# Optimization experiments

Measured on AMD Instinct MI355X. Metric: run time of the kernel, lower is better.

## Reference

```python
import jax, jax.numpy as jnp
import numpy as np

T, B, D = 4096, 64, 64
SCALE = D ** (-0.5)


def setup_inputs() -> dict:
    key = jax.random.key(0)
    ks = jax.random.split(key, 8)
    init = 1.0 / np.sqrt(D)  # mimic nn.Linear default scale roughly
    return {
        "eeg": jax.random.normal(ks[0], (T, B, D), dtype=jnp.float32),
        "fnirs": jax.random.normal(ks[1], (T, B, D), dtype=jnp.float32),
        "Wq": jax.random.normal(ks[2], (D, D), dtype=jnp.float32) * init,
        "bq": jax.random.normal(ks[3], (D,), dtype=jnp.float32) * init,
        "Wk": jax.random.normal(ks[4], (D, D), dtype=jnp.float32) * init,
        "bk": jax.random.normal(ks[5], (D,), dtype=jnp.float32) * init,
        "Wv": jax.random.normal(ks[6], (D, D), dtype=jnp.float32) * init,
        "bv": jax.random.normal(ks[7], (D,), dtype=jnp.float32) * init,
    }


def reference(eeg, fnirs, Wq, bq, Wk, bk, Wv, bv):
    # Linear layers: x @ W.T + b (torch nn.Linear convention, W is [out, in])
    q = jnp.einsum("tbd,od->tbo", eeg, Wq) + bq      # [T, B, D]
    k = jnp.einsum("tbd,od->tbo", fnirs, Wk) + bk    # [T, B, D]
    v = jnp.einsum("tbd,od->tbo", fnirs, Wv) + bv    # [T, B, D]
    # Elementwise QK gating score, summed over feature dim -> [T, B, 1]
    score = jnp.sum(q * k, axis=-1, keepdims=True) * SCALE
    # Softmax over the sequence axis (dim=0)
    attn = jax.nn.softmax(score, axis=0)
    # Residual combine
    return eeg + attn * v
```

## Files before the change

### kernel.cpp

```cpp
#include <hip/hip_runtime.h>
#include <hip/hip_bf16.h>
#include <math.h>

#define T_DIM 4096
#define B_DIM 64
#define D_DIM 64
#define NROWS (T_DIM * B_DIM)
#define NTILES (NROWS / 16)

#define WS_MBF   0
#define WS_VBF   2048
#define WS_UBF   4096
#define WS_W     4160
#define WS_C     4224
#define WS_SCORE 8192

typedef __attribute__((ext_vector_type(4))) float f32x4;
typedef __attribute__((ext_vector_type(8))) short bf16x8;

static __device__ inline short f2bf(float x) {
  __hip_bfloat16 h = __float2bfloat16(x);
  return *reinterpret_cast<short*>(&h);
}

static __device__ inline bf16x8 cvt8(const float4 a, const float4 b) {
  bf16x8 r;
  r[0] = f2bf(a.x); r[1] = f2bf(a.y); r[2] = f2bf(a.z); r[3] = f2bf(a.w);
  r[4] = f2bf(b.x); r[5] = f2bf(b.y); r[6] = f2bf(b.z); r[7] = f2bf(b.w);
  return r;
}

__global__ __launch_bounds__(64) void k1_precompute(
    const float* __restrict__ Wq, const float* __restrict__ bq,
    const float* __restrict__ Wk, const float* __restrict__ bk,
    const float* __restrict__ Wv, float* __restrict__ ws) {
  const int tid = threadIdx.x;
  const int blk = blockIdx.x;
  unsigned short* __restrict__ mbf = (unsigned short*)(ws + WS_MBF);
  unsigned short* __restrict__ vbf = (unsigned short*)(ws + WS_VBF);
  unsigned short* __restrict__ ubf = (unsigned short*)(ws + WS_UBF);
  if (blk < 64) {
    const int d = blk;
    float acc = 0.f;
    for (int o = 0; o < 64; ++o)
      acc = fmaf(Wq[o * 64 + d], Wk[o * 64 + tid], acc);
    mbf[d * 64 + tid] = (unsigned short)f2bf(acc);
    vbf[d * 64 + tid] = (unsigned short)f2bf(Wv[d * 64 + tid]);
  } else {
    float uacc = 0.f, wacc = 0.f, cacc = 0.f;
    for (int o = 0; o < 64; ++o) {
      uacc = fmaf(bq[o], Wk[o * 64 + tid], uacc);
      wacc = fmaf(Wq[o * 64 + tid], bk[o], wacc);
      cacc = fmaf(bq[o], bk[o], cacc);
    }
    ubf[tid] = (unsigned short)f2bf(uacc);
    ws[WS_W + tid] = wacc;
    if (tid == 0) ws[WS_C] = cacc;
  }
}

__global__ __launch_bounds__(256, 4) void k2_score_mfma(
    const float* __restrict__ eeg, const float* __restrict__ fnirs,
    const unsigned short* __restrict__ mbf, const float* __restrict__ wvec,
    const unsigned short* __restrict__ ubf, const float* __restrict__ cvec,
    float* __restrict__ score) {
  const int lane = threadIdx.x & 63;
  const int wv   = threadIdx.x >> 6;
  const int tile = blockIdx.x * 4 + wv;
  const int col  = lane & 15;
  const int grp  = lane >> 4;
  const int kb   = grp * 8;
  const int rbase = tile * 16;

  const float* fa = fnirs + (size_t)(rbase + col) * 64 + kb;
  const float4 f0a = *reinterpret_cast<const float4*>(fa);
  const float4 f0b = *reinterpret_cast<const float4*>(fa + 4);
  const float4 f1a = *reinterpret_cast<const float4*>(fa + 32);
  const float4 f1b = *reinterpret_cast<const float4*>(fa + 36);
  float ee[4][4];
#pragma unroll
  for (int i = 0; i < 4; ++i)
#pragma unroll
    for (int ct = 0; ct < 4; ++ct)
      ee[i][ct] = eeg[(size_t)(rbase + grp * 4 + i) * 64 + ct * 16 + col];

  bf16x8 bm[5][2];
#pragma unroll
  for (int ct = 0; ct < 4; ++ct)
#pragma unroll
    for (int kf = 0; kf < 2; ++kf)
      bm[ct][kf] = *reinterpret_cast<const bf16x8*>(
          mbf + (ct * 16 + col) * 64 + kf * 32 + kb);
#pragma unroll
  for (int kf = 0; kf < 2; ++kf) {
    bf16x8 z = (bf16x8)(short)0;
    if (col == 0)
      z = *reinterpret_cast<const bf16x8*>(ubf + kf * 32 + kb);
    bm[4][kf] = z;
  }
  const float wreg[4] = { wvec[col], wvec[16 + col], wvec[32 + col], wvec[48 + col] };
  const float cb = cvec[0];

  const bf16x8 a0 = cvt8(f0a, f0b);
  const bf16x8 a1 = cvt8(f1a, f1b);
  const f32x4 zero = {0.f, 0.f, 0.f, 0.f};
  f32x4 acc[5];
#pragma unroll
  for (int ct = 0; ct < 5; ++ct) {
    acc[ct] = __builtin_amdgcn_mfma_f32_16x16x32_bf16(a0, bm[ct][0], zero, 0, 0, 0);
    acc[ct] = __builtin_amdgcn_mfma_f32_16x16x32_bf16(a1, bm[ct][1], acc[ct], 0, 0, 0);
  }

  float partial[4];
#pragma unroll
  for (int i = 0; i < 4; ++i) {
    float s = 0.f;
#pragma unroll
    for (int ct = 0; ct < 4; ++ct)
      s = fmaf(ee[i][ct], acc[ct][i] + wreg[ct], s);
    if (col == 0) s += acc[4][i] + cb;
    partial[i] = s;
  }
#pragma unroll
  for (int m = 8; m >= 1; m >>= 1)
#pragma unroll
    for (int i = 0; i < 4; ++i)
      partial[i] += __shfl_xor(partial[i], m, 64);
  if (col == 0) {
    float4 o = { partial[0] * 0.125f, partial[1] * 0.125f,
                 partial[2] * 0.125f, partial[3] * 0.125f };
    *reinterpret_cast<float4*>(score + rbase + grp * 4) = o;
  }
}

__global__ __launch_bounds__(256) void k3_softmax(float* __restrict__ sc) {
  __shared__ float red[8];
  __shared__ float sinv;
  const int b = blockIdx.x;
  const int tid = threadIdx.x;

  float vals[16];
  float m = -1e30f;
#pragma unroll
  for (int k = 0; k < 16; ++k) {
    vals[k] = sc[(size_t)(k * 256 + tid) * 64 + b];
    m = fmaxf(m, vals[k]);
  }
#pragma unroll
  for (int off = 32; off > 0; off >>= 1)
    m = fmaxf(m, __shfl_xor(m, off, 64));
  if ((tid & 63) == 0) red[tid >> 6] = m;
  __syncthreads();
  m = fmaxf(fmaxf(red[0], red[1]), fmaxf(red[2], red[3]));

  float s = 0.f;
#pragma unroll
  for (int k = 0; k < 16; ++k) s += __expf(vals[k] - m);
#pragma unroll
  for (int off = 32; off > 0; off >>= 1)
    s += __shfl_xor(s, off, 64);
  if ((tid & 63) == 0) red[4 + (tid >> 6)] = s;
  __syncthreads();
  if (tid == 0) sinv = 1.0f / (red[4] + red[5] + red[6] + red[7]);
  __syncthreads();
  const float inv = sinv;
#pragma unroll
  for (int k = 0; k < 16; ++k)
    sc[(size_t)(k * 256 + tid) * 64 + b] = __expf(vals[k] - m) * inv;
}

__global__ __launch_bounds__(256, 4) void k4_output_mfma(
    const float* __restrict__ eeg, const float* __restrict__ fnirs,
    const unsigned short* __restrict__ vbf, const float* __restrict__ bv,
    const float* __restrict__ attn, float* __restrict__ out) {
  const int lane = threadIdx.x & 63;
  const int wv   = threadIdx.x >> 6;
  const int tile = blockIdx.x * 4 + wv;
  const int col  = lane & 15;
  const int grp  = lane >> 4;
  const int kb   = grp * 8;
  const int rbase = tile * 16;

  const float* fa = fnirs + (size_t)(rbase + col) * 64 + kb;
  const float4 f0a = *reinterpret_cast<const float4*>(fa);
  const float4 f0b = *reinterpret_cast<const float4*>(fa + 4);
  const float4 f1a = *reinterpret_cast<const float4*>(fa + 32);
  const float4 f1b = *reinterpret_cast<const float4*>(fa + 36);
  float ee[4][4];
#pragma unroll
  for (int i = 0; i < 4; ++i)
#pragma unroll
    for (int ct = 0; ct < 4; ++ct)
      ee[i][ct] = eeg[(size_t)(rbase + grp * 4 + i) * 64 + ct * 16 + col];
  const float4 a4 = *reinterpret_cast<const float4*>(attn + rbase + grp * 4);

  bf16x8 bm[4][2];
#pragma unroll
  for (int ct = 0; ct < 4; ++ct)
#pragma unroll
    for (int kf = 0; kf < 2; ++kf)
      bm[ct][kf] = *reinterpret_cast<const bf16x8*>(
          vbf + (ct * 16 + col) * 64 + kf * 32 + kb);
  const float bvreg[4] = { bv[col], bv[16 + col], bv[32 + col], bv[48 + col] };

  const bf16x8 a0 = cvt8(f0a, f0b);
  const bf16x8 a1 = cvt8(f1a, f1b);
  const f32x4 zero = {0.f, 0.f, 0.f, 0.f};
  f32x4 acc[4];
#pragma unroll
  for (int ct = 0; ct < 4; ++ct) {
    acc[ct] = __builtin_amdgcn_mfma_f32_16x16x32_bf16(a0, bm[ct][0], zero, 0, 0, 0);
    acc[ct] = __builtin_amdgcn_mfma_f32_16x16x32_bf16(a1, bm[ct][1], acc[ct], 0, 0, 0);
  }

  const float av[4] = { a4.x, a4.y, a4.z, a4.w };
#pragma unroll
  for (int i = 0; i < 4; ++i) {
    const size_t row = rbase + grp * 4 + i;
#pragma unroll
    for (int ct = 0; ct < 4; ++ct)
      out[row * 64 + ct * 16 + col] = fmaf(av[i], acc[ct][i] + bvreg[ct], ee[i][ct]);
  }
}

extern "C" void kernel_launch(void* const* d_in, const int* in_sizes, int n_in,
                              void* d_out, int out_size, void* d_ws, size_t ws_size,
                              hipStream_t stream) {
  const float* eeg   = (const float*)d_in[0];
  const float* fnirs = (const float*)d_in[1];
  const float* Wq    = (const float*)d_in[2];
  const float* bq    = (const float*)d_in[3];
  const float* Wk    = (const float*)d_in[4];
  const float* bk    = (const float*)d_in[5];
  const float* Wv    = (const float*)d_in[6];
  const float* bv    = (const float*)d_in[7];
  float* out = (float*)d_out;
  float* ws  = (float*)d_ws;

  k1_precompute<<<65, 64, 0, stream>>>(Wq, bq, Wk, bk, Wv, ws);
  k2_score_mfma<<<NTILES / 4, 256, 0, stream>>>(
      eeg, fnirs,
      (const unsigned short*)(ws + WS_MBF), ws + WS_W,
      (const unsigned short*)(ws + WS_UBF), ws + WS_C, ws + WS_SCORE);
  k3_softmax<<<64, 256, 0, stream>>>(ws + WS_SCORE);
  k4_output_mfma<<<NTILES / 4, 256, 0, stream>>>(
      eeg, fnirs, (const unsigned short*)(ws + WS_VBF), bv,
      ws + WS_SCORE, out);
}
```

Baseline: 79.63 us.

## Split softmax into parallel partial reductions and vectorize eeg/out access via transposed MFMA

The single 64-block softmax kernel becomes a 512-block online max/sum partial pass plus a tiny combine kernel. Normalization (exp and scale) moves into the output kernel, so the normalized attention no longer has to be written back. The MFMA operands are swapped so each lane owns one row and gets contiguous columns, which lets eeg loads and output stores use float4 and replaces the 16-lane shuffle reduction with two shuffles. The u bias term is now an fp32 dot product instead of an extra bf16 MFMA tile. The cost is one more kernel launch and one extra exp per row in the output kernel.

After: 87.48 us. +9.9%, slower.

```diff
diff --git a/kernel.cpp b/kernel.cpp
--- a/kernel.cpp
+++ b/kernel.cpp
@@ -10,9 +10,12 @@
 
 #define WS_MBF   0
 #define WS_VBF   2048
-#define WS_UBF   4096
+#define WS_U     4096
 #define WS_W     4160
 #define WS_C     4224
+#define WS_MX    4240
+#define WS_INV   4304
+#define WS_PART  4368
 #define WS_SCORE 8192
 
 typedef __attribute__((ext_vector_type(4))) float f32x4;
@@ -28,6 +31,12 @@
   r[0] = f2bf(a.x); r[1] = f2bf(a.y); r[2] = f2bf(a.z); r[3] = f2bf(a.w);
   r[4] = f2bf(b.x); r[5] = f2bf(b.y); r[6] = f2bf(b.z); r[7] = f2bf(b.w);
   return r;
+}
+
+static __device__ inline float dot4(const float4 a, const float4 b, float acc) {
+  acc = fmaf(a.x, b.x, acc); acc = fmaf(a.y, b.y, acc);
+  acc = fmaf(a.z, b.z, acc); acc = fmaf(a.w, b.w, acc);
+  return acc;
 }
 
 __global__ __launch_bounds__(64) void k1_precompute(
@@ -38,7 +47,6 @@
   const int blk = blockIdx.x;
   unsigned short* __restrict__ mbf = (unsigned short*)(ws + WS_MBF);
   unsigned short* __restrict__ vbf = (unsigned short*)(ws + WS_VBF);
-  unsigned short* __restrict__ ubf = (unsigned short*)(ws + WS_UBF);
   if (blk < 64) {
     const int d = blk;
     float acc = 0.f;
@@ -53,7 +61,7 @@
       wacc = fmaf(Wq[o * 64 + tid], bk[o], wacc);
       cacc = fmaf(bq[o], bk[o], cacc);
     }
-    ubf[tid] = (unsigned short)f2bf(uacc);
+    ws[WS_U + tid] = uacc;
     ws[WS_W + tid] = wacc;
     if (tid == 0) ws[WS_C] = cacc;
   }
@@ -62,7 +70,7 @@
 __global__ __launch_bounds__(256, 4) void k2_score_mfma(
     const float* __restrict__ eeg, const float* __restrict__ fnirs,
     const unsigned short* __restrict__ mbf, const float* __restrict__ wvec,
-    const unsigned short* __restrict__ ubf, const float* __restrict__ cvec,
+    const float* __restrict__ uvec, const float* __restrict__ cvec,
     float* __restrict__ score) {
   const int lane = threadIdx.x & 63;
   const int wv   = threadIdx.x >> 6;
@@ -77,102 +85,117 @@
   const float4 f0b = *reinterpret_cast<const float4*>(fa + 4);
   const float4 f1a = *reinterpret_cast<const float4*>(fa + 32);
   const float4 f1b = *reinterpret_cast<const float4*>(fa + 36);
-  float ee[4][4];
-#pragma unroll
-  for (int i = 0; i < 4; ++i)
-#pragma unroll
-    for (int ct = 0; ct < 4; ++ct)
-      ee[i][ct] = eeg[(size_t)(rbase + grp * 4 + i) * 64 + ct * 16 + col];
-
-  bf16x8 bm[5][2];
-#pragma unroll
-  for (int ct = 0; ct < 4; ++ct)
+  const float* ea = eeg + (size_t)(rbase + col) * 64 + grp * 4;
+  const float4 ef0 = *reinterpret_cast<const float4*>(ea);
+  const float4 ef1 = *reinterpret_cast<const float4*>(ea + 16);
+  const float4 ef2 = *reinterpret_cast<const float4*>(ea + 32);
+  const float4 ef3 = *reinterpret_cast<const float4*>(ea + 48);
+
+  bf16x8 bm[4][2];
+#pragma unroll
+  for (int dt = 0; dt < 4; ++dt)
 #pragma unroll
     for (int kf = 0; kf < 2; ++kf)
-      bm[ct][kf] = *reinterpret_cast<const bf16x8*>(
-          mbf + (ct * 16 + col) * 64 + kf * 32 + kb);
-#pragma unroll
-  for (int kf = 0; kf < 2; ++kf) {
-    bf16x8 z = (bf16x8)(short)0;
-    if (col == 0)
-      z = *reinterpret_cast<const bf16x8*>(ubf + kf * 32 + kb);
-    bm[4][kf] = z;
-  }
-  const float wreg[4] = { wvec[col], wvec[16 + col], wvec[32 + col], wvec[48 + col] };
+      bm[dt][kf] = *reinterpret_cast<const bf16x8*>(
+          mbf + (dt * 16 + col) * 64 + kf * 32 + kb);
+  const float4 wf0 = *reinterpret_cast<const float4*>(wvec + 0  + grp * 4);
+  const float4 wf1 = *reinterpret_cast<const float4*>(wvec + 16 + grp * 4);
+  const float4 wf2 = *reinterpret_cast<const float4*>(wvec + 32 + grp * 4);
+  const float4 wf3 = *reinterpret_cast<const float4*>(wvec + 48 + grp * 4);
+  const float4 u0a = *reinterpret_cast<const float4*>(uvec + kb);
+  const float4 u0b = *reinterpret_cast<const float4*>(uvec + kb + 4);
+  const float4 u1a = *reinterpret_cast<const float4*>(uvec + kb + 32);
+  const float4 u1b = *reinterpret_cast<const float4*>(uvec + kb + 36);
   const float cb = cvec[0];
+
+  float s = 0.f;
+  s = dot4(f0a, u0a, s); s = dot4(f0b, u0b, s);
+  s = dot4(f1a, u1a, s); s = dot4(f1b, u1b, s);
 
   const bf16x8 a0 = cvt8(f0a, f0b);
   const bf16x8 a1 = cvt8(f1a, f1b);
   const f32x4 zero = {0.f, 0.f, 0.f, 0.f};
-  f32x4 acc[5];
-#pragma unroll
-  for (int ct = 0; ct < 5; ++ct) {
-    acc[ct] = __builtin_amdgcn_mfma_f32_16x16x32_bf16(a0, bm[ct][0], zero, 0, 0, 0);
-    acc[ct] = __builtin_amdgcn_mfma_f32_16x16x32_bf16(a1, bm[ct][1], acc[ct], 0, 0, 0);
-  }
-
-  float partial[4];
-#pragma unroll
-  for (int i = 0; i < 4; ++i) {
-    float s = 0.f;
-#pragma unroll
-    for (int ct = 0; ct < 4; ++ct)
-      s = fmaf(ee[i][ct], acc[ct][i] + wreg[ct], s);
-    if (col == 0) s += acc[4][i] + cb;
-    partial[i] = s;
-  }
-#pragma unroll
-  for (int m = 8; m >= 1; m >>= 1)
-#pragma unroll
-    for (int i = 0; i < 4; ++i)
-      partial[i] += __shfl_xor(partial[i], m, 64);
-  if (col == 0) {
-    float4 o = { partial[0] * 0.125f, partial[1] * 0.125f,
-                 partial[2] * 0.125f, partial[3] * 0.125f };
-    *reinterpret_cast<float4*>(score + rbase + grp * 4) = o;
-  }
-}
-
-__global__ __launch_bounds__(256) void k3_softmax(float* __restrict__ sc) {
-  __shared__ float red[8];
-  __shared__ float sinv;
-  const int b = blockIdx.x;
+  f32x4 acc[4];
+#pragma unroll
+  for (int dt = 0; dt < 4; ++dt) {
+    acc[dt] = __builtin_amdgcn_mfma_f32_16x16x32_bf16(bm[dt][0], a0, zero, 0, 0, 0);
+    acc[dt] = __builtin_amdgcn_mfma_f32_16x16x32_bf16(bm[dt][1], a1, acc[dt], 0, 0, 0);
+  }
+
+  float4 h;
+  h.x = acc[0][0] + wf0.x; h.y = acc[0][1] + wf0.y; h.z = acc[0][2] + wf0.z; h.w = acc[0][3] + wf0.w;
+  s = dot4(ef0, h, s);
+  h.x = acc[1][0] + wf1.x; h.y = acc[1][1] + wf1.y; h.z = acc[1][2] + wf1.z; h.w = acc[1][3] + wf1.w;
+  s = dot4(ef1, h, s);
+  h.x = acc[2][0] + wf2.x; h.y = acc[2][1] + wf2.y; h.z = acc[2][2] + wf2.z; h.w = acc[2][3] + wf2.w;
+  s = dot4(ef2, h, s);
+  h.x = acc[3][0] + wf3.x; h.y = acc[3][1] + wf3.y; h.z = acc[3][2] + wf3.z; h.w = acc[3][3] + wf3.w;
+  s = dot4(ef3, h, s);
+
+  s += __shfl_xor(s, 16, 64);
+  s += __shfl_xor(s, 32, 64);
+  if (lane < 16)
+    score[rbase + lane] = (s + cb) * 0.125f;
+}
+
+__global__ __launch_bounds__(256) void k3a_partial(
+    const float* __restrict__ sc, float* __restrict__ part) {
+  __shared__ float lm[4], ls[4];
+  const int bi = blockIdx.x;
+  const int b  = bi >> 3;
+  const int ck = bi & 7;
   const int tid = threadIdx.x;
-
-  float vals[16];
-  float m = -1e30f;
-#pragma unroll
-  for (int k = 0; k < 16; ++k) {
-    vals[k] = sc[(size_t)(k * 256 + tid) * 64 + b];
-    m = fmaxf(m, vals[k]);
-  }
-#pragma unroll
-  for (int off = 32; off > 0; off >>= 1)
-    m = fmaxf(m, __shfl_xor(m, off, 64));
-  if ((tid & 63) == 0) red[tid >> 6] = m;
+  const int t0 = ck * 512;
+
+  const float v1 = sc[(size_t)(t0 + tid) * 64 + b];
+  const float v2 = sc[(size_t)(t0 + 256 + tid) * 64 + b];
+  float m = fmaxf(v1, v2);
+  float s = __expf(v1 - m) + __expf(v2 - m);
+#pragma unroll
+  for (int off = 32; off > 0; off >>= 1) {
+    const float mo = __shfl_xor(m, off, 64);
+    const float so = __shfl_xor(s, off, 64);
+    const float mn = fmaxf(m, mo);
+    s = s * __expf(m - mn) + so * __expf(mo - mn);
+    m = mn;
+  }
+  if ((tid & 63) == 0) { lm[tid >> 6] = m; ls[tid >> 6] = s; }
   __syncthreads();
-  m = fmaxf(fmaxf(red[0], red[1]), fmaxf(red[2], red[3]));
-
-  float s = 0.f;
-#pragma unroll
-  for (int k = 0; k < 16; ++k) s += __expf(vals[k] - m);
-#pragma unroll
-  for (int off = 32; off > 0; off >>= 1)
-    s += __shfl_xor(s, off, 64);
-  if ((tid & 63) == 0) red[4 + (tid >> 6)] = s;
-  __syncthreads();
-  if (tid == 0) sinv = 1.0f / (red[4] + red[5] + red[6] + red[7]);
-  __syncthreads();
-  const float inv = sinv;
-#pragma unroll
-  for (int k = 0; k < 16; ++k)
-    sc[(size_t)(k * 256 + tid) * 64 + b] = __expf(vals[k] - m) * inv;
+  if (tid == 0) {
+    float M = lm[0], S = ls[0];
+#pragma unroll
+    for (int w = 1; w < 4; ++w) {
+      const float Mn = fmaxf(M, lm[w]);
+      S = S * __expf(M - Mn) + ls[w] * __expf(lm[w] - Mn);
+      M = Mn;
+    }
+    part[bi * 2] = M;
+    part[bi * 2 + 1] = S;
+  }
+}
+
+__global__ __launch_bounds__(64) void k3b_combine(
+    const float* __restrict__ part, float* __restrict__ mx,
+    float* __restrict__ inv) {
+  const int b = threadIdx.x;
+  float M = part[(b * 8) * 2], S = part[(b * 8) * 2 + 1];
+#pragma unroll
+  for (int ck = 1; ck < 8; ++ck) {
+    const float m2 = part[(b * 8 + ck) * 2];
+    const float s2 = part[(b * 8 + ck) * 2 + 1];
+    const float Mn = fmaxf(M, m2);
+    S = S * __expf(M - Mn) + s2 * __expf(m2 - Mn);
+    M = Mn;
+  }
+  mx[b] = M;
+  inv[b] = 1.0f / S;
 }
 
 __global__ __launch_bounds__(256, 4) void k4_output_mfma(
     const float* __restrict__ eeg, const float* __restrict__ fnirs,
     const unsigned short* __restrict__ vbf, const float* __restrict__ bv,
-    const float* __restrict__ attn, float* __restrict__ out) {
+    const float* __restrict__ score, const float* __restrict__ mx,
+    const float* __restrict__ inv, float* __restrict__ out) {
   const int lane = threadIdx.x & 63;
   const int wv   = threadIdx.x >> 6;
   const int tile = blockIdx.x * 4 + wv;
@@ -180,47 +203,57 @@
   const int grp  = lane >> 4;
   const int kb   = grp * 8;
   const int rbase = tile * 16;
-
-  const float* fa = fnirs + (size_t)(rbase + col) * 64 + kb;
+  const int r = rbase + col;
+  const int b = r & 63;
+
+  const float* fa = fnirs + (size_t)r * 64 + kb;
   const float4 f0a = *reinterpret_cast<const float4*>(fa);
   const float4 f0b = *reinterpret_cast<const float4*>(fa + 4);
   const float4 f1a = *reinterpret_cast<const float4*>(fa + 32);
   const float4 f1b = *reinterpret_cast<const float4*>(fa + 36);
-  float ee[4][4];
-#pragma unroll
-  for (int i = 0; i < 4; ++i)
-#pragma unroll
-    for (int ct = 0; ct < 4; ++ct)
-      ee[i][ct] = eeg[(size_t)(rbase + grp * 4 + i) * 64 + ct * 16 + col];
-  const float4 a4 = *reinterpret_cast<const float4*>(attn + rbase + grp * 4);
+  const float* ea = eeg + (size_t)r * 64 + grp * 4;
+  const float4 ef0 = *reinterpret_cast<const float4*>(ea);
+  const float4 ef1 = *reinterpret_cast<const float4*>(ea + 16);
+  const float4 ef2 = *reinterpret_cast<const float4*>(ea + 32);
+  const float4 ef3 = *reinterpret_cast<const float4*>(ea + 48);
+  const float a = __expf(score[r] - mx[b]) * inv[b];
 
   bf16x8 bm[4][2];
 #pragma unroll
-  for (int ct = 0; ct < 4; ++ct)
+  for (int dt = 0; dt < 4; ++dt)
 #pragma unroll
     for (int kf = 0; kf < 2; ++kf)
-      bm[ct][kf] = *reinterpret_cast<const bf16x8*>(
-          vbf + (ct * 16 + col) * 64 + kf * 32 + kb);
-  const float bvreg[4] = { bv[col], bv[16 + col], bv[32 + col], bv[48 + col] };
+      bm[dt][kf] = *reinterpret_cast<const bf16x8*>(
+          vbf + (dt * 16 + col) * 64 + kf * 32 + kb);
+  const float4 bv0 = *reinterpret_cast<const float4*>(bv + 0  + grp * 4);
+  const float4 bv1 = *reinterpret_cast<const float4*>(bv + 16 + grp * 4);
+  const float4 bv2 = *reinterpret_cast<const float4*>(bv + 32 + grp * 4);
+  const float4 bv3 = *reinterpret_cast<const float4*>(bv + 48 + grp * 4);
 
   const bf16x8 a0 = cvt8(f0a, f0b);
   const bf16x8 a1 = cvt8(f1a, f1b);
   const f32x4 zero = {0.f, 0.f, 0.f, 0.f};
   f32x4 acc[4];
 #pragma unroll
-  for (int ct = 0; ct < 4; ++ct) {
-    acc[ct] = __builtin_amdgcn_mfma_f32_16x16x32_bf16(a0, bm[ct][0], zero, 0, 0, 0);
-    acc[ct] = __builtin_amdgcn_mfma_f32_16x16x32_bf16(a1, bm[ct][1], acc[ct], 0, 0, 0);
-  }
-
-  const float av[4] = { a4.x, a4.y, a4.z, a4.w };
-#pragma unroll
-  for (int i = 0; i < 4; ++i) {
-    const size_t row = rbase + grp * 4 + i;
-#pragma unroll
-    for (int ct = 0; ct < 4; ++ct)
-      out[row * 64 + ct * 16 + col] = fmaf(av[i], acc[ct][i] + bvreg[ct], ee[i][ct]);
-  }
+  for (int dt = 0; dt < 4; ++dt) {
+    acc[dt] = __builtin_amdgcn_mfma_f32_16x16x32_bf16(bm[dt][0], a0, zero, 0, 0, 0);
+    acc[dt] = __builtin_amdgcn_mfma_f32_16x16x32_bf16(bm[dt][1], a1, acc[dt], 0, 0, 0);
+  }
+
+  float* oa = out + (size_t)r * 64 + grp * 4;
+  float4 o;
+  o.x = fmaf(a, acc[0][0] + bv0.x, ef0.x); o.y = fmaf(a, acc[0][1] + bv0.y, ef0.y);
+  o.z = fmaf(a, acc[0][2] + bv0.z, ef0.z); o.w = fmaf(a, acc[0][3] + bv0.w, ef0.w);
+  *reinterpret_cast<float4*>(oa) = o;
+  o.x = fmaf(a, acc[1][0] + bv1.x, ef1.x); o.y = fmaf(a, acc[1][1] + bv1.y, ef1.y);
+  o.z = fmaf(a, acc[1][2] + bv1.z, ef1.z); o.w = fmaf(a, acc[1][3] + bv1.w, ef1.w);
+  *reinterpret_cast<float4*>(oa + 16) = o;
+  o.x = fmaf(a, acc[2][0] + bv2.x, ef2.x); o.y = fmaf(a, acc[2][1] + bv2.y, ef2.y);
+  o.z = fmaf(a, acc[2][2] + bv2.z, ef2.z); o.w = fmaf(a, acc[2][3] + bv2.w, ef2.w);
+  *reinterpret_cast<float4*>(oa + 32) = o;
+  o.x = fmaf(a, acc[3][0] + bv3.x, ef3.x); o.y = fmaf(a, acc[3][1] + bv3.y, ef3.y);
+  o.z = fmaf(a, acc[3][2] + bv3.z, ef3.z); o.w = fmaf(a, acc[3][3] + bv3.w, ef3.w);
+  *reinterpret_cast<float4*>(oa + 48) = o;
 }
 
 extern "C" void kernel_launch(void* const* d_in, const int* in_sizes, int n_in,
@@ -239,11 +272,11 @@
 
   k1_precompute<<<65, 64, 0, stream>>>(Wq, bq, Wk, bk, Wv, ws);
   k2_score_mfma<<<NTILES / 4, 256, 0, stream>>>(
-      eeg, fnirs,
-      (const unsigned short*)(ws + WS_MBF), ws + WS_W,
-      (const unsigned short*)(ws + WS_UBF), ws + WS_C, ws + WS_SCORE);
-  k3_softmax<<<64, 256, 0, stream>>>(ws + WS_SCORE);
+      eeg, fnirs, (const unsigned short*)(ws + WS_MBF), ws + WS_W,
+      ws + WS_U, ws + WS_C, ws + WS_SCORE);
+  k3a_partial<<<512, 256, 0, stream>>>(ws + WS_SCORE, ws + WS_PART);
+  k3b_combine<<<1, 64, 0, stream>>>(ws + WS_PART, ws + WS_MX, ws + WS_INV);
   k4_output_mfma<<<NTILES / 4, 256, 0, stream>>>(
       eeg, fnirs, (const unsigned short*)(ws + WS_VBF), bv,
-      ws + WS_SCORE, out);
-}
+      ws + WS_SCORE, ws + WS_MX, ws + WS_INV, out);
+}
```
